# Performance work log

Measured on AMD Instinct MI355X. Metric: run time of the kernel, lower is better.

## Reference

```python
import jax, jax.numpy as jnp
import numpy as np

EPS = 1e-7  # entropy eps
DIAG_EPS = 1e-8
LEAK = 0.2  # LeakyReLU slope


def _entropy(p):
    # EntropyLoss: mean over leading dims of -sum(p*log(p+eps), -1)
    return jnp.mean(-jnp.sum(p * jnp.log(p + EPS), axis=-1))


def setup_inputs() -> dict:
    key = jax.random.key(0)
    ks = jax.random.split(key, 7)
    B, S, C, F, E, H = 256, 6, 80, 2048, 300, 1024
    x = jax.random.normal(ks[0], (B, F, 14, 14), dtype=jnp.float32)
    inp = jax.random.normal(ks[1], (C, E), dtype=jnp.float32) * 0.1
    y = (jax.random.uniform(ks[2], (B, C)) < 0.1).astype(jnp.float32)
    # persistent co-occurrence buffer (non-negative counts)
    comatrix = jax.random.uniform(ks[3], (S, C, C), dtype=jnp.float32) * 50.0
    W_scene = jax.random.normal(ks[4], (F, S), dtype=jnp.float32) * 0.02
    W1 = jax.random.uniform(ks[5], (E, H), dtype=jnp.float32, minval=-1, maxval=1) / np.sqrt(H)
    W2 = jax.random.uniform(ks[6], (H, F), dtype=jnp.float32, minval=-1, maxval=1) / np.sqrt(F)
    return {"x": x, "inp": inp, "y": y, "comatrix": comatrix,
            "W_scene": W_scene, "W1": W1, "W2": W2}


def reference(x, inp, y, comatrix, W_scene, W1, W2):
    B = x.shape[0]
    S, C, _ = comatrix.shape
    # backbone output -> MaxPool2d(14,14) == global max over the 14x14 map
    img_feats = jnp.max(x, axis=(2, 3))                       # [B, F]
    scene_scores = img_feats @ W_scene                        # [B, S]
    scene_probs = jax.nn.softmax(scene_scores, axis=-1)
    # --- training-path comatrix scatter update (comat_smooth=False) ---
    batch_comats = y[:, :, None] * y[:, None, :]              # [B, C, C]
    ids = jnp.argmax(scene_probs, axis=-1)                    # [B]
    comatrix = comatrix + jnp.zeros_like(comatrix).at[ids].add(batch_comats)
    # --- entropy terms ---
    sample_en = _entropy(scene_probs)
    max_en = _entropy(jnp.full((S,), 1.0 / S, dtype=scene_probs.dtype))
    batch_en = (max_en - _entropy(jnp.mean(scene_probs, axis=0))) * 100.0
    # --- comatrix2prob: row-normalize by diagonal, force diag=1 ---
    diag = jnp.diagonal(comatrix, axis1=1, axis2=2)[:, :, None]  # [S, C, 1]
    comat = comatrix / (diag + DIAG_EPS)
    eye = jnp.eye(C, dtype=comat.dtype)
    comat = comat * (1.0 - eye) + eye
    comats = comat[ids]                                       # gather [B, C, C]
    # --- gen_adj: adj = D^{-1/2} A^T D^{-1/2}, D = rowsums(A) ---
    D = jax.lax.rsqrt(jnp.sum(comats, axis=2))                # [B, C]
    adjs = D[:, :, None] * jnp.swapaxes(comats, 1, 2) * D[:, None, :]
    # --- 2-layer GCN ---
    h = adjs @ (inp @ W1)                                     # [B, C, 1024]
    h = jnp.where(h > 0, h, LEAK * h)
    h = adjs @ (h @ W2)                                       # [B, C, 2048]
    output = jnp.einsum('bcf,bf->bc', h, img_feats)           # [B, C]
    return (output, scene_probs, sample_en, batch_en, comats)
```

## Files before the change

### kernel.cpp

```cpp
#include <hip/hip_runtime.h>
#include <math.h>

#define B_ 256
#define S_ 6
#define C_ 80
#define F_ 2048
#define E_ 300
#define H_ 1024
#define EPS_ 1e-7f
#define DEPS_ 1e-8f
#define LEAK_ 0.2f

#define IMG_OFF   0u
#define Z_OFF     524288u
#define COMAT_OFF 606208u
#define ADJA_OFF  644608u
#define G_OFF     683008u
#define PART_OFF  1174528u
#define IDS_OFF   5368832u

#define OUT0_OFF 0
#define PROB_OFF 20480
#define SEN_OUT  22016
#define BEN_OUT  22017
#define CMTS_OFF 22018

__global__ __launch_bounds__(256) void k_pool_z(const float* __restrict__ x,
                                                float* __restrict__ img,
                                                const float* __restrict__ inp,
                                                const float* __restrict__ W1,
                                                float* __restrict__ Z) {
    if (blockIdx.x < 320) {
        int c = blockIdx.x >> 2;
        int h = ((blockIdx.x & 3) << 8) + threadIdx.x;
        float acc = 0.f;
        for (int e = 0; e < E_; e++) acc += inp[c * E_ + e] * W1[e * H_ + h];
        Z[c * H_ + h] = acc;
    } else {
        int pair = (blockIdx.x - 320) * 4 + (threadIdx.x >> 6);
        int lane = threadIdx.x & 63;
        const float4* xp = (const float4*)x + (size_t)pair * 49;
        float m = -INFINITY;
        if (lane < 49) {
            float4 v = xp[lane];
            m = fmaxf(fmaxf(v.x, v.y), fmaxf(v.z, v.w));
        }
#pragma unroll
        for (int off = 32; off >= 1; off >>= 1) m = fmaxf(m, __shfl_xor(m, off));
        if (lane == 0) img[pair] = m;
    }
}

__global__ __launch_bounds__(256) void k_scene_ugemm(const float* __restrict__ img,
                                                     const float* __restrict__ Ws,
                                                     const float* __restrict__ W2,
                                                     float* __restrict__ probs_out,
                                                     int* __restrict__ ids,
                                                     float* __restrict__ part) {
    __shared__ float sm[2 * 16 * 132];
    int tid = threadIdx.x;
    if (blockIdx.x < 256) {
        float (*red)[256] = (float(*)[256])sm;
        int b = blockIdx.x;
        float acc[6] = {0, 0, 0, 0, 0, 0};
#pragma unroll
        for (int i = 0; i < 8; i++) {
            int f = tid + i * 256;
            float a = img[b * F_ + f];
#pragma unroll
            for (int s = 0; s < 6; s++) acc[s] += a * Ws[f * 6 + s];
        }
        for (int s = 0; s < 6; s++) red[s][tid] = acc[s];
        __syncthreads();
        for (int off = 128; off > 0; off >>= 1) {
            if (tid < off)
                for (int s = 0; s < 6; s++) red[s][tid] += red[s][tid + off];
            __syncthreads();
        }
        if (tid == 0) {
            float sc[6], mx = -INFINITY;
            for (int s = 0; s < 6; s++) { sc[s] = red[s][0]; mx = fmaxf(mx, sc[s]); }
            float sum = 0.f;
            for (int s = 0; s < 6; s++) { sc[s] = expf(sc[s] - mx); sum += sc[s]; }
            float inv = 1.0f / sum;
            int best = 0; float bv = -1.f;
            for (int s = 0; s < 6; s++) {
                float p = sc[s] * inv;
                probs_out[b * 6 + s] = p;
                if (p > bv) { bv = p; best = s; }
            }
            ids[b] = best;
        }
    } else {
        float* As = sm;
        float* Bs = sm + 16 * 132;
        int t = blockIdx.x - 256;
        int bx = t & 7, by = (t >> 3) & 1, bz = t >> 4;
        int m0 = by * 128, h0 = bx * 128;
        int kbase = bz * 128;
        float acc[8][8];
#pragma unroll
        for (int i = 0; i < 8; i++)
#pragma unroll
            for (int j = 0; j < 8; j++) acc[i][j] = 0.f;
        int r0 = (tid >> 4) << 3, c0 = (tid & 15) << 3;
        for (int st = 0; st < 8; st++) {
            int kc = kbase + st * 16;
#pragma unroll
            for (int l = 0; l < 2; l++) {
                int fid = tid + (l << 8);
                int r = fid >> 2, kq = fid & 3;
                float4 av = *(const float4*)(img + (size_t)(m0 + r) * 2048 + kc + (kq << 2));
                float4 bv = *(const float4*)(W2 + (size_t)(h0 + r) * 2048 + kc + (kq << 2));
                int kk = kq << 2;
                As[(kk + 0) * 132 + r] = av.x; As[(kk + 1) * 132 + r] = av.y;
                As[(kk + 2) * 132 + r] = av.z; As[(kk + 3) * 132 + r] = av.w;
                Bs[(kk + 0) * 132 + r] = bv.x; Bs[(kk + 1) * 132 + r] = bv.y;
                Bs[(kk + 2) * 132 + r] = bv.z; Bs[(kk + 3) * 132 + r] = bv.w;
            }
            __syncthreads();
#pragma unroll
            for (int k = 0; k < 16; k++) {
                float4 a0 = *(const float4*)&As[k * 132 + r0];
                float4 a1 = *(const float4*)&As[k * 132 + r0 + 4];
                float4 b0 = *(const float4*)&Bs[k * 132 + c0];
                float4 b1 = *(const float4*)&Bs[k * 132 + c0 + 4];
                float ar[8] = {a0.x, a0.y, a0.z, a0.w, a1.x, a1.y, a1.z, a1.w};
                float br[8] = {b0.x, b0.y, b0.z, b0.w, b1.x, b1.y, b1.z, b1.w};
#pragma unroll
                for (int i = 0; i < 8; i++)
#pragma unroll
                    for (int j = 0; j < 8; j++) acc[i][j] += ar[i] * br[j];
            }
            __syncthreads();
        }
        float* pu = part + (size_t)bz * 262144;
#pragma unroll
        for (int i = 0; i < 8; i++) {
            int row = m0 + r0 + i;
            float4 v0 = {acc[i][0], acc[i][1], acc[i][2], acc[i][3]};
            float4 v1 = {acc[i][4], acc[i][5], acc[i][6], acc[i][7]};
            *(float4*)(pu + (size_t)row * 1024 + h0 + c0) = v0;
            *(float4*)(pu + (size_t)row * 1024 + h0 + c0 + 4) = v1;
        }
    }
}

__global__ __launch_bounds__(256) void k_comat(const float* __restrict__ y,
                                               const float* __restrict__ cm_in,
                                               const int* __restrict__ ids,
                                               float* __restrict__ comat,
                                               float* __restrict__ adjA) {
    int s = blockIdx.x, tid = threadIdx.x;
    __shared__ unsigned long long colq[80][4];
    __shared__ float cm[6400];
    __shared__ float diag[80], Dn[80];
    __shared__ int idsL[256];
    idsL[tid] = ids[tid];
    __syncthreads();
    int wave = tid >> 6, lane = tid & 63;
    int b = tid;
    bool ok = (idsL[b] == s);
    for (int i = 0; i < 80; i++) {
        bool pred = ok && (y[b * 80 + i] != 0.0f);
        unsigned long long mk = __ballot(pred);
        if (lane == 0) colq[i][wave] = mk;
    }
    __syncthreads();
    for (int p = tid; p < 6400; p += 256) {
        int i = p / 80, j = p - i * 80;
        int cnt = 0;
#pragma unroll
        for (int w = 0; w < 4; w++) cnt += __popcll(colq[i][w] & colq[j][w]);
        cm[p] = cm_in[s * 6400 + p] + (float)cnt;
    }
    __syncthreads();
    if (tid < 80) diag[tid] = cm[tid * 81];
    __syncthreads();
    for (int p = tid; p < 6400; p += 256) {
        int i = p / 80, j = p - i * 80;
        float v = (i == j) ? 1.0f : cm[p] / (diag[i] + DEPS_);
        cm[p] = v;
        comat[s * 6400 + p] = v;
    }
    __syncthreads();
    if (tid < 80) {
        float rs = 0.f;
        for (int j = 0; j < 80; j++) rs += cm[tid * 80 + j];
        Dn[tid] = 1.0f / sqrtf(rs);
    }
    __syncthreads();
    for (int p = tid; p < 6400; p += 256) {
        int i = p / 80, j = p - i * 80;
        adjA[s * 6400 + p] = Dn[i] * cm[j * 80 + i] * Dn[j];
    }
}

__global__ __launch_bounds__(256) void k_g_gather(const float* __restrict__ adjA,
                                                  const float* __restrict__ Z,
                                                  float* __restrict__ g,
                                                  const float* __restrict__ comat,
                                                  const int* __restrict__ ids,
                                                  float* __restrict__ cmts) {
    if (blockIdx.x < 480) {
        int s = blockIdx.x / 80, c = blockIdx.x % 80;
        const float* row = adjA + (s * 80 + c) * 80;
        const float4* Z4 = (const float4*)Z;
        float4 acc = {0, 0, 0, 0};
        for (int j = 0; j < 80; j++) {
            float a = row[j];
            float4 z = Z4[j * 256 + threadIdx.x];
            acc.x += a * z.x; acc.y += a * z.y; acc.z += a * z.z; acc.w += a * z.w;
        }
        acc.x = acc.x > 0.f ? acc.x : LEAK_ * acc.x;
        acc.y = acc.y > 0.f ? acc.y : LEAK_ * acc.y;
        acc.z = acc.z > 0.f ? acc.z : LEAK_ * acc.z;
        acc.w = acc.w > 0.f ? acc.w : LEAK_ * acc.w;
        ((float4*)g)[(s * 80 + c) * 256 + threadIdx.x] = acc;
    } else {
        int b = blockIdx.x - 480;
        int s = ids[b];
        const float2* src = (const float2*)(comat + s * 6400);
        float2* dst = (float2*)(cmts + (size_t)b * 6400);
        for (int i = threadIdx.x; i < 3200; i += 256) dst[i] = src[i];
    }
}

__global__ __launch_bounds__(320) void k_out_final(const float* __restrict__ part,
                                                   const float* __restrict__ g,
                                                   const float* __restrict__ adjA,
                                                   const int* __restrict__ ids,
                                                   const float* __restrict__ probs,
                                                   float* __restrict__ out0,
                                                   float* __restrict__ o_sen,
                                                   float* __restrict__ o_ben) {
    __shared__ float ul[1024];
    __shared__ float tp[320];
    __shared__ float tv[80];
    int tid = threadIdx.x;
    if (blockIdx.x == 256) {
        if (tid < 64) {
            float lent = 0.f;
            float lp[6] = {0, 0, 0, 0, 0, 0};
            for (int i = 0; i < 4; i++) {
                int b = tid * 4 + i;
#pragma unroll
                for (int s = 0; s < 6; s++) {
                    float p = probs[b * 6 + s];
                    lp[s] += p;
                    lent -= p * logf(p + EPS_);
                }
            }
#pragma unroll
            for (int off = 32; off >= 1; off >>= 1) {
                lent += __shfl_xor(lent, off);
#pragma unroll
                for (int s = 0; s < 6; s++) lp[s] += __shfl_xor(lp[s], off);
            }
            if (tid == 0) {
                *o_sen = lent / 256.0f;
                float ent = 0.f;
                for (int s = 0; s < 6; s++) {
                    float q = lp[s] / 256.0f;
                    ent -= q * logf(q + EPS_);
                }
                float invS = 1.0f / 6.0f;
                float men = -6.0f * (invS * logf(invS + EPS_));
                *o_ben = (men - ent) * 100.0f;
            }
        }
        return;
    }
    int b = blockIdx.x;
    int s = ids[b];
    for (int h = tid; h < 1024; h += 320) {
        float a = 0.f;
#pragma unroll
        for (int z = 0; z < 16; z++) a += part[z * 262144 + b * 1024 + h];
        ul[h] = a;
    }
    __syncthreads();
    int c = tid >> 2, q = tid & 3;
    const float4* gp = (const float4*)(g + (s * 80 + c) * 1024 + q * 256);
    const float4* up = (const float4*)(ul + q * 256);
    float a = 0.f;
    for (int k = 0; k < 64; k++) {
        float4 gv = gp[k];
        float4 uv = up[k];
        a += gv.x * uv.x + gv.y * uv.y + gv.z * uv.z + gv.w * uv.w;
    }
    tp[tid] = a;
    __syncthreads();
    if (tid < 80) tv[tid] = tp[tid * 4] + tp[tid * 4 + 1] + tp[tid * 4 + 2] + tp[tid * 4 + 3];
    __syncthreads();
    if (tid < 80) {
        const float* ar = adjA + (s * 80 + tid) * 80;
        float o = 0.f;
        for (int j = 0; j < 80; j++) o += ar[j] * tv[j];
        out0[b * 80 + tid] = o;
    }
}

extern "C" void kernel_launch(void* const* d_in, const int* in_sizes, int n_in,
                              void* d_out, int out_size, void* d_ws, size_t ws_size,
                              hipStream_t stream) {
    const float* x    = (const float*)d_in[0];
    const float* inp  = (const float*)d_in[1];
    const float* y    = (const float*)d_in[2];
    const float* cmin = (const float*)d_in[3];
    const float* Ws   = (const float*)d_in[4];
    const float* W1   = (const float*)d_in[5];
    const float* W2   = (const float*)d_in[6];
    float* out = (float*)d_out;
    float* W = (float*)d_ws;

    float* img   = W + IMG_OFF;
    float* Z     = W + Z_OFF;
    float* comat = W + COMAT_OFF;
    float* adjA  = W + ADJA_OFF;
    float* g     = W + G_OFF;
    float* part  = W + PART_OFF;
    int*   ids   = (int*)(W + IDS_OFF);

    k_pool_z<<<131392, 256, 0, stream>>>(x, img, inp, W1, Z);
    k_scene_ugemm<<<512, 256, 0, stream>>>(img, Ws, W2, out + PROB_OFF, ids, part);
    k_comat<<<6, 256, 0, stream>>>(y, cmin, ids, comat, adjA);
    k_g_gather<<<736, 256, 0, stream>>>(adjA, Z, g, comat, ids, out + CMTS_OFF);
    k_out_final<<<257, 320, 0, stream>>>(part, g, adjA, ids, out + PROB_OFF,
                                         out + OUT0_OFF, out + SEN_OUT, out + BEN_OUT);
}
```

Measured before the change: 626.8 us.

## Fuse comat build into graph kernel and halve split-K partitions of U GEMM

Merges the comatrix build, adjacency computation, gather copy and entropy reduction into one kernel in which every block redundantly rebuilds its scene's normalized comatrix in shared memory. This removes one launch and the serial 6-block comat kernel. The U GEMM split-K goes from 16 to 8 slices, so there are fewer partial buffers to sum, at the cost of fewer GEMM blocks and longer per-block K loops. The trade is heavy duplicated work per block, with about 736 blocks each recomputing an 80x80 matrix and ballot pass.

```diff
diff --git a/kernel.cpp b/kernel.cpp
--- a/kernel.cpp
+++ b/kernel.cpp
@@ -13,7 +13,6 @@
 
 #define IMG_OFF   0u
 #define Z_OFF     524288u
-#define COMAT_OFF 606208u
 #define ADJA_OFF  644608u
 #define G_OFF     683008u
 #define PART_OFF  1174528u
@@ -97,14 +96,14 @@
         int t = blockIdx.x - 256;
         int bx = t & 7, by = (t >> 3) & 1, bz = t >> 4;
         int m0 = by * 128, h0 = bx * 128;
-        int kbase = bz * 128;
+        int kbase = bz * 256;
         float acc[8][8];
 #pragma unroll
         for (int i = 0; i < 8; i++)
 #pragma unroll
             for (int j = 0; j < 8; j++) acc[i][j] = 0.f;
         int r0 = (tid >> 4) << 3, c0 = (tid & 15) << 3;
-        for (int st = 0; st < 8; st++) {
+        for (int st = 0; st < 16; st++) {
             int kc = kbase + st * 16;
 #pragma unroll
             for (int l = 0; l < 2; l++) {
@@ -146,99 +145,18 @@
     }
 }
 
-__global__ __launch_bounds__(256) void k_comat(const float* __restrict__ y,
+__global__ __launch_bounds__(256) void k_graph(const float* __restrict__ y,
                                                const float* __restrict__ cm_in,
                                                const int* __restrict__ ids,
-                                               float* __restrict__ comat,
-                                               float* __restrict__ adjA) {
-    int s = blockIdx.x, tid = threadIdx.x;
-    __shared__ unsigned long long colq[80][4];
-    __shared__ float cm[6400];
-    __shared__ float diag[80], Dn[80];
-    __shared__ int idsL[256];
-    idsL[tid] = ids[tid];
-    __syncthreads();
-    int wave = tid >> 6, lane = tid & 63;
-    int b = tid;
-    bool ok = (idsL[b] == s);
-    for (int i = 0; i < 80; i++) {
-        bool pred = ok && (y[b * 80 + i] != 0.0f);
-        unsigned long long mk = __ballot(pred);
-        if (lane == 0) colq[i][wave] = mk;
-    }
-    __syncthreads();
-    for (int p = tid; p < 6400; p += 256) {
-        int i = p / 80, j = p - i * 80;
-        int cnt = 0;
-#pragma unroll
-        for (int w = 0; w < 4; w++) cnt += __popcll(colq[i][w] & colq[j][w]);
-        cm[p] = cm_in[s * 6400 + p] + (float)cnt;
-    }
-    __syncthreads();
-    if (tid < 80) diag[tid] = cm[tid * 81];
-    __syncthreads();
-    for (int p = tid; p < 6400; p += 256) {
-        int i = p / 80, j = p - i * 80;
-        float v = (i == j) ? 1.0f : cm[p] / (diag[i] + DEPS_);
-        cm[p] = v;
-        comat[s * 6400 + p] = v;
-    }
-    __syncthreads();
-    if (tid < 80) {
-        float rs = 0.f;
-        for (int j = 0; j < 80; j++) rs += cm[tid * 80 + j];
-        Dn[tid] = 1.0f / sqrtf(rs);
-    }
-    __syncthreads();
-    for (int p = tid; p < 6400; p += 256) {
-        int i = p / 80, j = p - i * 80;
-        adjA[s * 6400 + p] = Dn[i] * cm[j * 80 + i] * Dn[j];
-    }
-}
-
-__global__ __launch_bounds__(256) void k_g_gather(const float* __restrict__ adjA,
-                                                  const float* __restrict__ Z,
-                                                  float* __restrict__ g,
-                                                  const float* __restrict__ comat,
-                                                  const int* __restrict__ ids,
-                                                  float* __restrict__ cmts) {
-    if (blockIdx.x < 480) {
-        int s = blockIdx.x / 80, c = blockIdx.x % 80;
-        const float* row = adjA + (s * 80 + c) * 80;
-        const float4* Z4 = (const float4*)Z;
-        float4 acc = {0, 0, 0, 0};
-        for (int j = 0; j < 80; j++) {
-            float a = row[j];
-            float4 z = Z4[j * 256 + threadIdx.x];
-            acc.x += a * z.x; acc.y += a * z.y; acc.z += a * z.z; acc.w += a * z.w;
-        }
-        acc.x = acc.x > 0.f ? acc.x : LEAK_ * acc.x;
-        acc.y = acc.y > 0.f ? acc.y : LEAK_ * acc.y;
-        acc.z = acc.z > 0.f ? acc.z : LEAK_ * acc.z;
-        acc.w = acc.w > 0.f ? acc.w : LEAK_ * acc.w;
-        ((float4*)g)[(s * 80 + c) * 256 + threadIdx.x] = acc;
-    } else {
-        int b = blockIdx.x - 480;
-        int s = ids[b];
-        const float2* src = (const float2*)(comat + s * 6400);
-        float2* dst = (float2*)(cmts + (size_t)b * 6400);
-        for (int i = threadIdx.x; i < 3200; i += 256) dst[i] = src[i];
-    }
-}
-
-__global__ __launch_bounds__(320) void k_out_final(const float* __restrict__ part,
-                                                   const float* __restrict__ g,
-                                                   const float* __restrict__ adjA,
-                                                   const int* __restrict__ ids,
-                                                   const float* __restrict__ probs,
-                                                   float* __restrict__ out0,
-                                                   float* __restrict__ o_sen,
-                                                   float* __restrict__ o_ben) {
-    __shared__ float ul[1024];
-    __shared__ float tp[320];
-    __shared__ float tv[80];
+                                               const float* __restrict__ Z,
+                                               const float* __restrict__ probs,
+                                               float* __restrict__ adjA,
+                                               float* __restrict__ g,
+                                               float* __restrict__ cmts,
+                                               float* __restrict__ o_sen,
+                                               float* __restrict__ o_ben) {
     int tid = threadIdx.x;
-    if (blockIdx.x == 256) {
+    if (blockIdx.x == 736) {
         if (tid < 64) {
             float lent = 0.f;
             float lp[6] = {0, 0, 0, 0, 0, 0};
@@ -271,12 +189,84 @@
         }
         return;
     }
-    int b = blockIdx.x;
+    __shared__ unsigned long long colq[80][4];
+    __shared__ float cm[6400];
+    __shared__ float diag[80], Dn[80], arow[80];
+    __shared__ int idsL[256];
+    bool isG = blockIdx.x < 480;
+    int s, c = 0, b = 0;
+    if (isG) { s = blockIdx.x / 80; c = blockIdx.x % 80; }
+    else { b = blockIdx.x - 480; s = ids[b]; }
+    idsL[tid] = ids[tid];
+    __syncthreads();
+    int wave = tid >> 6, lane = tid & 63;
+    bool ok = (idsL[tid] == s);
+    for (int i = 0; i < 80; i++) {
+        unsigned long long mk = __ballot(ok && (y[tid * 80 + i] != 0.0f));
+        if (lane == 0) colq[i][wave] = mk;
+    }
+    __syncthreads();
+    for (int p = tid; p < 6400; p += 256) {
+        int i = p / 80, j = p - i * 80;
+        int cnt = 0;
+#pragma unroll
+        for (int w = 0; w < 4; w++) cnt += __popcll(colq[i][w] & colq[j][w]);
+        cm[p] = cm_in[s * 6400 + p] + (float)cnt;
+    }
+    __syncthreads();
+    if (tid < 80) diag[tid] = cm[tid * 81];
+    __syncthreads();
+    for (int p = tid; p < 6400; p += 256) {
+        int i = p / 80, j = p - i * 80;
+        cm[p] = (i == j) ? 1.0f : cm[p] / (diag[i] + DEPS_);
+    }
+    __syncthreads();
+    if (!isG) {
+        const float2* src = (const float2*)cm;
+        float2* dst = (float2*)(cmts + (size_t)b * 6400);
+        for (int i = tid; i < 3200; i += 256) dst[i] = src[i];
+        return;
+    }
+    if (tid < 80) {
+        float rs = 0.f;
+        for (int j = 0; j < 80; j++) rs += cm[tid * 80 + j];
+        Dn[tid] = 1.0f / sqrtf(rs);
+    }
+    __syncthreads();
+    if (tid < 80) {
+        float v = Dn[c] * cm[tid * 80 + c] * Dn[tid];
+        arow[tid] = v;
+        adjA[(s * 80 + c) * 80 + tid] = v;
+    }
+    __syncthreads();
+    const float4* Z4 = (const float4*)Z;
+    float4 acc = {0, 0, 0, 0};
+    for (int j = 0; j < 80; j++) {
+        float a = arow[j];
+        float4 z = Z4[j * 256 + tid];
+        acc.x += a * z.x; acc.y += a * z.y; acc.z += a * z.z; acc.w += a * z.w;
+    }
+    acc.x = acc.x > 0.f ? acc.x : LEAK_ * acc.x;
+    acc.y = acc.y > 0.f ? acc.y : LEAK_ * acc.y;
+    acc.z = acc.z > 0.f ? acc.z : LEAK_ * acc.z;
+    acc.w = acc.w > 0.f ? acc.w : LEAK_ * acc.w;
+    ((float4*)g)[(s * 80 + c) * 256 + tid] = acc;
+}
+
+__global__ __launch_bounds__(320) void k_out(const float* __restrict__ part,
+                                             const float* __restrict__ g,
+                                             const float* __restrict__ adjA,
+                                             const int* __restrict__ ids,
+                                             float* __restrict__ out0) {
+    __shared__ float ul[1024];
+    __shared__ float tp[320];
+    __shared__ float tv[80];
+    int b = blockIdx.x, tid = threadIdx.x;
     int s = ids[b];
     for (int h = tid; h < 1024; h += 320) {
         float a = 0.f;
 #pragma unroll
-        for (int z = 0; z < 16; z++) a += part[z * 262144 + b * 1024 + h];
+        for (int z = 0; z < 8; z++) a += part[z * 262144 + b * 1024 + h];
         ul[h] = a;
     }
     __syncthreads();
@@ -316,16 +306,14 @@
 
     float* img   = W + IMG_OFF;
     float* Z     = W + Z_OFF;
-    float* comat = W + COMAT_OFF;
     float* adjA  = W + ADJA_OFF;
     float* g     = W + G_OFF;
     float* part  = W + PART_OFF;
     int*   ids   = (int*)(W + IDS_OFF);
 
     k_pool_z<<<131392, 256, 0, stream>>>(x, img, inp, W1, Z);
-    k_scene_ugemm<<<512, 256, 0, stream>>>(img, Ws, W2, out + PROB_OFF, ids, part);
-    k_comat<<<6, 256, 0, stream>>>(y, cmin, ids, comat, adjA);
-    k_g_gather<<<736, 256, 0, stream>>>(adjA, Z, g, comat, ids, out + CMTS_OFF);
-    k_out_final<<<257, 320, 0, stream>>>(part, g, adjA, ids, out + PROB_OFF,
-                                         out + OUT0_OFF, out + SEN_OUT, out + BEN_OUT);
-}
+    k_scene_ugemm<<<384, 256, 0, stream>>>(img, Ws, W2, out + PROB_OFF, ids, part);
+    k_graph<<<737, 256, 0, stream>>>(y, cmin, ids, Z, out + PROB_OFF, adjA, g,
+                                     out + CMTS_OFF, out + SEN_OUT, out + BEN_OUT);
+    k_out<<<256, 320, 0, stream>>>(part, g, adjA, ids, out + OUT0_OFF);
+}
```

New measurement: 632.4 us. No clear change (+0.9%).
